# Performance work log

Measured on AMD Instinct MI355X. Metric: run time of the kernel, lower is better.

Reference implementation:

```python
import jax, jax.numpy as jnp
import numpy as np

B, S, DIM, DA = 64, 4096, 256, 64
NEG = -1e30

def setup_inputs() -> dict:
    key = jax.random.key(0)
    k1, k2, k3, k4 = jax.random.split(key, 4)
    h = jax.random.normal(k1, (B, S, DIM), dtype=jnp.float32)
    mask = jax.random.randint(k2, (B, S), 0, 2).astype(jnp.bool_)
    # xavier_uniform with gain=1.414 as in the torch module
    lim_a = 1.414 * np.sqrt(6.0 / (DIM + DA))
    lim_b = 1.414 * np.sqrt(6.0 / (DA + 1))
    a = jax.random.uniform(k3, (DIM, DA), minval=-lim_a, maxval=lim_a, dtype=jnp.float32)
    b = jax.random.uniform(k4, (DA, 1), minval=-lim_b, maxval=lim_b, dtype=jnp.float32)
    return {"h": h, "mask": mask, "a": a, "b": b}

def reference(h, mask, a, b):
    # e: (B, S) additive-attention logits
    e = jnp.einsum('bsk,ko->bs', jnp.tanh(jnp.einsum('bsd,dk->bsk', h, a)), b)
    e = e + mask.astype(e.dtype) * NEG  # True == padding -> -1e30
    attn = jax.nn.softmax(e, axis=1)    # softmax over seq dim
    # weighted sum over seq: (B, DIM)
    return jnp.einsum('bs,bsd->bd', attn, h)
```

## Files before the change

kernel.cpp:

```cpp
#include <hip/hip_runtime.h>
#include <hip/hip_bf16.h>

#define B_    64
#define S_    4096
#define DIM_  256
#define DA_   64
#define NEG_  (-1e30f)

typedef __attribute__((ext_vector_type(8))) short short8;
typedef __attribute__((ext_vector_type(4))) float float4v;

static __device__ inline unsigned short f2bf(float x) {
    union { float f; unsigned u; } v; v.f = x;
    unsigned r = v.u + 0x7fffu + ((v.u >> 16) & 1u);
    return (unsigned short)(r >> 16);
}

__global__ __launch_bounds__(256) void prep_kernel(
    const float* __restrict__ a, const void* __restrict__ mask,
    unsigned short* __restrict__ at, int* __restrict__ flag)
{
    int idx = blockIdx.x * 256 + threadIdx.x;
    int k = idx >> 8;
    int d = idx & 255;
    at[k * DIM_ + d] = f2bf(a[d * DA_ + k]);

    if (blockIdx.x == 0) {
        __shared__ int anynz;
        if (threadIdx.x == 0) anynz = 0;
        __syncthreads();
        const unsigned char* mb = (const unsigned char*)mask;
        int base = threadIdx.x * 4;
        int v = mb[base + 1] | mb[base + 2] | mb[base + 3];
        if (v) atomicOr(&anynz, 1);
        __syncthreads();
        if (threadIdx.x == 0) *flag = (anynz == 0) ? 1 : 0;
    }
}

__global__ __launch_bounds__(256) void logits_kernel(
    const float* __restrict__ h, const unsigned short* __restrict__ at,
    const float* __restrict__ bvec, float* __restrict__ e)
{
    __shared__ unsigned short hs[64 * 264];
    const int t = threadIdx.x;
    const long long s0 = (long long)blockIdx.x * 64;
    const float* hblk = h + s0 * DIM_;

    #pragma unroll
    for (int j = 0; j < 16; ++j) {
        int f = t + j * 256;
        int row = f >> 6;
        int col = (f & 63) * 4;
        float4 v = *(const float4*)(hblk + row * DIM_ + col);
        unsigned b0 = f2bf(v.x), b1 = f2bf(v.y), b2 = f2bf(v.z), b3 = f2bf(v.w);
        uint2 packed;
        packed.x = b0 | (b1 << 16);
        packed.y = b2 | (b3 << 16);
        *(uint2*)&hs[row * 264 + col] = packed;
    }
    __syncthreads();

    const int wave = t >> 6;
    const int lane = t & 63;
    const int quad = lane >> 4;
    const int nrow = lane & 15;

    float4v acc[4];
    #pragma unroll
    for (int nt = 0; nt < 4; ++nt) acc[nt] = (float4v){0.f, 0.f, 0.f, 0.f};

    const unsigned short* hrow = &hs[(wave * 16 + nrow) * 264];
    #pragma unroll
    for (int kb = 0; kb < 8; ++kb) {
        short8 afrag = *(const short8*)(hrow + kb * 32 + quad * 8);
        #pragma unroll
        for (int nt = 0; nt < 4; ++nt) {
            short8 bfrag = *(const short8*)(at + (nt * 16 + nrow) * DIM_ + kb * 32 + quad * 8);
            acc[nt] = __builtin_amdgcn_mfma_f32_16x16x32_bf16(afrag, bfrag, acc[nt], 0, 0, 0);
        }
    }

    float bv[4];
    #pragma unroll
    for (int nt = 0; nt < 4; ++nt) bv[nt] = bvec[nt * 16 + nrow];

    #pragma unroll
    for (int r = 0; r < 4; ++r) {
        float p = 0.f;
        #pragma unroll
        for (int nt = 0; nt < 4; ++nt) p += tanhf(acc[nt][r]) * bv[nt];
        p += __shfl_xor(p, 1);
        p += __shfl_xor(p, 2);
        p += __shfl_xor(p, 4);
        p += __shfl_xor(p, 8);
        if (nrow == r)
            e[s0 + wave * 16 + quad * 4 + r] = p;
    }
}

__global__ __launch_bounds__(1024) void softmax_kernel(
    float* __restrict__ e, const void* __restrict__ mask, const int* __restrict__ flag)
{
    const int b = blockIdx.x;
    const int t = threadIdx.x;
    const bool int32enc = (*flag != 0);
    const long long base = (long long)b * S_;

    float ev[4];
    #pragma unroll
    for (int i = 0; i < 4; ++i) {
        int s = t + i * 1024;
        float x = e[base + s];
        int m;
        if (int32enc) m = ((const int*)mask)[base + s];
        else          m = ((const unsigned char*)mask)[base + s];
        ev[i] = m ? NEG_ : x;
    }

    __shared__ float red[16];
    float mx = fmaxf(fmaxf(ev[0], ev[1]), fmaxf(ev[2], ev[3]));
    #pragma unroll
    for (int off = 32; off >= 1; off >>= 1) mx = fmaxf(mx, __shfl_xor(mx, off));
    if ((t & 63) == 0) red[t >> 6] = mx;
    __syncthreads();
    float m = red[0];
    #pragma unroll
    for (int i = 1; i < 16; ++i) m = fmaxf(m, red[i]);
    __syncthreads();

    float ex[4];
    float l = 0.f;
    #pragma unroll
    for (int i = 0; i < 4; ++i) { ex[i] = __expf(ev[i] - m); l += ex[i]; }
    #pragma unroll
    for (int off = 32; off >= 1; off >>= 1) l += __shfl_xor(l, off);
    if ((t & 63) == 0) red[t >> 6] = l;
    __syncthreads();
    float lt = 0.f;
    #pragma unroll
    for (int i = 0; i < 16; ++i) lt += red[i];

    float inv = 1.0f / lt;
    #pragma unroll
    for (int i = 0; i < 4; ++i) e[base + t + i * 1024] = ex[i] * inv;
}

__global__ __launch_bounds__(256) void wsum_kernel(
    const float* __restrict__ h, const float* __restrict__ w, float* __restrict__ out)
{
    const int b = blockIdx.x >> 4;
    const int c = blockIdx.x & 15;
    const int t = threadIdx.x;
    __shared__ float wch[256];
    const long long s0 = (long long)b * S_ + c * 256;
    wch[t] = w[s0 + t];
    __syncthreads();

    const float* hb = h + s0 * DIM_;
    float acc = 0.f;
    #pragma unroll 8
    for (int i = 0; i < 256; ++i)
        acc = fmaf(wch[i], hb[(size_t)i * DIM_ + t], acc);
    atomicAdd(&out[b * DIM_ + t], acc);
}

extern "C" void kernel_launch(void* const* d_in, const int* in_sizes, int n_in,
                              void* d_out, int out_size, void* d_ws, size_t ws_size,
                              hipStream_t stream) {
    const float* h    = (const float*)d_in[0];
    const void*  mask = d_in[1];
    const float* a    = (const float*)d_in[2];
    const float* bvec = (const float*)d_in[3];
    float* out = (float*)d_out;

    char* ws = (char*)d_ws;
    unsigned short* at = (unsigned short*)ws;
    int* flag          = (int*)(ws + 32768);
    float* e           = (float*)(ws + 36864);

    hipMemsetAsync(d_out, 0, (size_t)B_ * DIM_ * sizeof(float), stream);
    prep_kernel<<<64, 256, 0, stream>>>(a, mask, at, flag);
    logits_kernel<<<(B_ * S_) / 64, 256, 0, stream>>>(h, at, bvec, e);
    softmax_kernel<<<B_, 1024, 0, stream>>>(e, mask, flag);
    wsum_kernel<<<B_ * 16, 256, 0, stream>>>(h, e, out);
}
```

Measured before the change: 448.8 us.

## Stage fp16 copy of h for weighted sum and pre-swizzle MFMA B operand

The logits kernel now also writes an fp16 copy of h while it converts the tile to bf16. The weighted-sum kernel then reads that half-width copy with vectorized 4-element loads, splits each 512-row chunk across waves and reduces the partial sums in shared memory. The intent is to halve the bytes the second pass reads. The cost is an extra global write of the same size, so total traffic barely changes, and the weighted sum is now computed from fp16 values of h, which loses precision. Separately, the projection matrix is stored pre-swizzled in MFMA fragment order so each lane's B-fragment load is contiguous and coalesced.

```diff
diff --git a/kernel.cpp b/kernel.cpp
--- a/kernel.cpp
+++ b/kernel.cpp
@@ -18,12 +18,17 @@
 
 __global__ __launch_bounds__(256) void prep_kernel(
     const float* __restrict__ a, const void* __restrict__ mask,
-    unsigned short* __restrict__ at, int* __restrict__ flag)
+    unsigned short* __restrict__ at_sw, int* __restrict__ flag)
 {
     int idx = blockIdx.x * 256 + threadIdx.x;
-    int k = idx >> 8;
-    int d = idx & 255;
-    at[k * DIM_ + d] = f2bf(a[d * DA_ + k]);
+    int j    = idx & 7;
+    int lane = (idx >> 3) & 63;
+    int kbnt = idx >> 9;
+    int kb   = kbnt & 7;
+    int nt   = kbnt >> 3;
+    int d  = kb * 32 + (lane >> 4) * 8 + j;
+    int kf = nt * 16 + (lane & 15);
+    at_sw[idx] = f2bf(a[d * DA_ + kf]);
 
     if (blockIdx.x == 0) {
         __shared__ int anynz;
@@ -39,25 +44,37 @@
 }
 
 __global__ __launch_bounds__(256) void logits_kernel(
-    const float* __restrict__ h, const unsigned short* __restrict__ at,
-    const float* __restrict__ bvec, float* __restrict__ e)
+    const float* __restrict__ h, const unsigned short* __restrict__ at_sw,
+    const float* __restrict__ bvec, float* __restrict__ e,
+    unsigned short* __restrict__ h16)
 {
     __shared__ unsigned short hs[64 * 264];
     const int t = threadIdx.x;
     const long long s0 = (long long)blockIdx.x * 64;
     const float* hblk = h + s0 * DIM_;
-
-    #pragma unroll
-    for (int j = 0; j < 16; ++j) {
-        int f = t + j * 256;
-        int row = f >> 6;
-        int col = (f & 63) * 4;
-        float4 v = *(const float4*)(hblk + row * DIM_ + col);
-        unsigned b0 = f2bf(v.x), b1 = f2bf(v.y), b2 = f2bf(v.z), b3 = f2bf(v.w);
-        uint2 packed;
-        packed.x = b0 | (b1 << 16);
-        packed.y = b2 | (b3 << 16);
-        *(uint2*)&hs[row * 264 + col] = packed;
+    unsigned short* h16blk = h16 + s0 * DIM_;
+
+    #pragma unroll
+    for (int j = 0; j < 8; ++j) {
+        int f2 = t + j * 256;
+        int row = f2 >> 5;
+        int col = (f2 & 31) * 8;
+        const float* src = hblk + row * DIM_ + col;
+        float4 v0 = *(const float4*)(src);
+        float4 v1 = *(const float4*)(src + 4);
+        uint2 p0, p1;
+        p0.x = f2bf(v0.x) | ((unsigned)f2bf(v0.y) << 16);
+        p0.y = f2bf(v0.z) | ((unsigned)f2bf(v0.w) << 16);
+        p1.x = f2bf(v1.x) | ((unsigned)f2bf(v1.y) << 16);
+        p1.y = f2bf(v1.z) | ((unsigned)f2bf(v1.w) << 16);
+        *(uint2*)&hs[row * 264 + col]     = p0;
+        *(uint2*)&hs[row * 264 + col + 4] = p1;
+        union { _Float16 hh[8]; uint4 u; } pk;
+        pk.hh[0] = (_Float16)v0.x; pk.hh[1] = (_Float16)v0.y;
+        pk.hh[2] = (_Float16)v0.z; pk.hh[3] = (_Float16)v0.w;
+        pk.hh[4] = (_Float16)v1.x; pk.hh[5] = (_Float16)v1.y;
+        pk.hh[6] = (_Float16)v1.z; pk.hh[7] = (_Float16)v1.w;
+        *(uint4*)(h16blk + (size_t)f2 * 8) = pk.u;
     }
     __syncthreads();
 
@@ -76,7 +93,7 @@
         short8 afrag = *(const short8*)(hrow + kb * 32 + quad * 8);
         #pragma unroll
         for (int nt = 0; nt < 4; ++nt) {
-            short8 bfrag = *(const short8*)(at + (nt * 16 + nrow) * DIM_ + kb * 32 + quad * 8);
+            short8 bfrag = *(const short8*)(at_sw + ((nt * 8 + kb) * 64 + lane) * 8);
             acc[nt] = __builtin_amdgcn_mfma_f32_16x16x32_bf16(afrag, bfrag, acc[nt], 0, 0, 0);
         }
     }
@@ -147,22 +164,43 @@
 }
 
 __global__ __launch_bounds__(256) void wsum_kernel(
-    const float* __restrict__ h, const float* __restrict__ w, float* __restrict__ out)
-{
-    const int b = blockIdx.x >> 4;
-    const int c = blockIdx.x & 15;
+    const unsigned short* __restrict__ h16, const float* __restrict__ w,
+    float* __restrict__ out)
+{
+    const int b = blockIdx.x >> 3;
+    const int c = blockIdx.x & 7;
     const int t = threadIdx.x;
-    __shared__ float wch[256];
-    const long long s0 = (long long)b * S_ + c * 256;
-    wch[t] = w[s0 + t];
-    __syncthreads();
-
-    const float* hb = h + s0 * DIM_;
-    float acc = 0.f;
-    #pragma unroll 8
-    for (int i = 0; i < 256; ++i)
-        acc = fmaf(wch[i], hb[(size_t)i * DIM_ + t], acc);
-    atomicAdd(&out[b * DIM_ + t], acc);
+    const int wv = t >> 6;
+    const int col = (t & 63) * 4;
+
+    __shared__ float wch[512];
+    __shared__ float red[4 * 256];
+    const int sbase = c * 512;
+    wch[t]       = w[(long long)b * S_ + sbase + t];
+    wch[t + 256] = w[(long long)b * S_ + sbase + t + 256];
+    __syncthreads();
+
+    const unsigned short* hb = h16 + ((long long)b * S_ + sbase) * DIM_;
+    float a0 = 0.f, a1 = 0.f, a2 = 0.f, a3 = 0.f;
+    #pragma unroll 4
+    for (int i = 0; i < 128; ++i) {
+        int s = i * 4 + wv;
+        union { ushort4 u; _Float16 hh[4]; } pk;
+        pk.u = *(const ushort4*)(hb + (size_t)s * DIM_ + col);
+        float wt = wch[s];
+        a0 = fmaf(wt, (float)pk.hh[0], a0);
+        a1 = fmaf(wt, (float)pk.hh[1], a1);
+        a2 = fmaf(wt, (float)pk.hh[2], a2);
+        a3 = fmaf(wt, (float)pk.hh[3], a3);
+    }
+    red[wv * 256 + col + 0] = a0;
+    red[wv * 256 + col + 1] = a1;
+    red[wv * 256 + col + 2] = a2;
+    red[wv * 256 + col + 3] = a3;
+    __syncthreads();
+
+    float sum = red[t] + red[256 + t] + red[512 + t] + red[768 + t];
+    atomicAdd(&out[b * DIM_ + t], sum);
 }
 
 extern "C" void kernel_launch(void* const* d_in, const int* in_sizes, int n_in,
@@ -175,13 +213,14 @@
     float* out = (float*)d_out;
 
     char* ws = (char*)d_ws;
-    unsigned short* at = (unsigned short*)ws;
-    int* flag          = (int*)(ws + 32768);
-    float* e           = (float*)(ws + 36864);
+    unsigned short* at_sw = (unsigned short*)ws;
+    int* flag             = (int*)(ws + 32768);
+    float* e              = (float*)(ws + 36864);
+    unsigned short* h16   = (unsigned short*)(ws + 1085440);
 
     hipMemsetAsync(d_out, 0, (size_t)B_ * DIM_ * sizeof(float), stream);
-    prep_kernel<<<64, 256, 0, stream>>>(a, mask, at, flag);
-    logits_kernel<<<(B_ * S_) / 64, 256, 0, stream>>>(h, at, bvec, e);
+    prep_kernel<<<64, 256, 0, stream>>>(a, mask, at_sw, flag);
+    logits_kernel<<<(B_ * S_) / 64, 256, 0, stream>>>(h, at_sw, bvec, e, h16);
     softmax_kernel<<<B_, 1024, 0, stream>>>(e, mask, flag);
-    wsum_kernel<<<B_ * 16, 256, 0, stream>>>(h, e, out);
-}
+    wsum_kernel<<<B_ * 8, 256, 0, stream>>>(h16, e, out);
+}
```

After: 420.9 us. -6.2%, faster.
